# Kernel tuning notes

Hardware: AMD Instinct MI355X
Metric: run time of the kernel (lower is better)

The kernel has to match this reference:

```python
import jax, jax.numpy as jnp
import numpy as np

SPARSITY = 0.1
B, N, K = 256, 65536, 64

def setup_inputs() -> dict:
    key = jax.random.key(0)
    kx, kc = jax.random.split(key)
    x = jax.random.normal(kx, (B, N), dtype=jnp.float32)
    cluster_assignments = jax.random.randint(kc, (N,), 0, K, dtype=jnp.int32)
    cluster_weights = jnp.ones((K,), dtype=jnp.float32)
    return {"x": x, "cluster_weights": cluster_weights, "cluster_assignments": cluster_assignments}

def reference(x, cluster_weights, cluster_assignments):
    b, n = x.shape
    k = cluster_weights.shape[0]
    # cluster activation prob (context=None path): softmax(weights), same for all batch rows
    p = jax.nn.softmax(cluster_weights) * SPARSITY                      # [K]
    ku, kv = jax.random.split(jax.random.key(42))
    u = jax.random.uniform(ku, (b, n))   # drives the random permutation per (batch, cluster)
    v = jax.random.uniform(kv, (b, n))   # drives the binomial count (sum of Bernoullis)
    # Binomial(len(cluster_i), p_i) == sum of per-neuron Bernoulli(p_i) over the cluster
    bern = (v < p[cluster_assignments][None, :]).astype(jnp.int32)      # [B, N]
    counts = jax.vmap(lambda row: jax.ops.segment_sum(row, cluster_assignments, num_segments=k))(bern)  # [B, K]
    counts = jnp.maximum(counts, 1)                                     # max(1, binomial sample)
    # within-cluster uniform-random ranking: sort by (cluster, u); rank = pos - cluster_start
    sizes = jnp.bincount(cluster_assignments, length=k)                 # [K]
    starts = jnp.cumsum(sizes) - sizes                                  # exclusive cumsum [K]
    cluster_sorted = jnp.sort(cluster_assignments)                      # [N], batch-independent
    pos_in_cluster = jnp.arange(n) - starts[cluster_sorted]             # [N]
    keys = cluster_assignments.astype(jnp.float32)[None, :] + u * 0.999  # cluster-major composite key
    order = jnp.argsort(keys, axis=1)                                   # [B, N]
    mask_sorted = (pos_in_cluster[None, :] < counts[:, cluster_sorted]).astype(x.dtype)  # [B, N]
    mask = jnp.zeros_like(x).at[jnp.arange(b)[:, None], order].set(mask_sorted)
    return x * mask
```

## Files before the change

kernel.cpp:

```cpp
#include <hip/hip_runtime.h>
#include <stdint.h>

#define NROWS 256
#define NCOLS 65536
#define KCL   64
#define TMAX  20
#define NBLK  128
#define CHUNK (NCOLS / NBLK)
#define ZBLK  2048

__device__ __forceinline__ void tf2x32(uint32_t k0, uint32_t k1,
                                       uint32_t x0, uint32_t x1,
                                       uint32_t& o0, uint32_t& o1) {
  const uint32_t ks2 = k0 ^ k1 ^ 0x1BD11BDAu;
  x0 += k0; x1 += k1;
#define TFR(r) { x0 += x1; x1 = __builtin_rotateleft32(x1, (r)); x1 ^= x0; }
  TFR(13) TFR(15) TFR(26) TFR(6)
  x0 += k1; x1 += ks2 + 1u;
  TFR(17) TFR(29) TFR(16) TFR(24)
  x0 += ks2; x1 += k0 + 2u;
  TFR(13) TFR(15) TFR(26) TFR(6)
  x0 += k0; x1 += k1 + 3u;
  TFR(17) TFR(29) TFR(16) TFR(24)
  x0 += k1; x1 += ks2 + 4u;
  TFR(13) TFR(15) TFR(26) TFR(6)
  x0 += ks2; x1 += k0 + 5u;
#undef TFR
  o0 = x0; o1 = x1;
}

__device__ __forceinline__ uint32_t jax_bits(uint32_t k0, uint32_t k1, uint32_t f) {
  uint32_t o0, o1;
  tf2x32(k0, k1, 0u, f, o0, o1);
  return o0 ^ o1;
}

__device__ __forceinline__ float bits_to_u01(uint32_t bits) {
  return __uint_as_float((bits >> 9) | 0x3f800000u) - 1.0f;
}

__device__ __forceinline__ float key_from_ubits(uint32_t ubits, float kf) {
  return __fadd_rn(kf, __fmul_rn(bits_to_u01(ubits), 0.999f));
}

__device__ __forceinline__ int wave_sum_i(int v) {
  v += __builtin_amdgcn_update_dpp(0, v, 0xB1,  0xF, 0xF, true);
  v += __builtin_amdgcn_update_dpp(0, v, 0x4E,  0xF, 0xF, true);
  v += __builtin_amdgcn_update_dpp(0, v, 0x141, 0xF, 0xF, true);
  v += __builtin_amdgcn_update_dpp(0, v, 0x140, 0xF, 0xF, true);
  v += __builtin_amdgcn_ds_swizzle(v, 0x401F);
  v += __shfl_xor(v, 32, 64);
  return v;
}
__device__ __forceinline__ uint32_t wave_min_u(uint32_t v) {
  uint32_t o;
  o = (uint32_t)__builtin_amdgcn_update_dpp(0, (int)v, 0xB1,  0xF, 0xF, true); v = (o < v) ? o : v;
  o = (uint32_t)__builtin_amdgcn_update_dpp(0, (int)v, 0x4E,  0xF, 0xF, true); v = (o < v) ? o : v;
  o = (uint32_t)__builtin_amdgcn_update_dpp(0, (int)v, 0x141, 0xF, 0xF, true); v = (o < v) ? o : v;
  o = (uint32_t)__builtin_amdgcn_update_dpp(0, (int)v, 0x140, 0xF, 0xF, true); v = (o < v) ? o : v;
  o = (uint32_t)__builtin_amdgcn_ds_swizzle((int)v, 0x401F);                   v = (o < v) ? o : v;
  o = (uint32_t)__shfl_xor((int)v, 32, 64);                                    v = (o < v) ? o : v;
  return v;
}
__device__ __forceinline__ int wave_min_i(int v) {
  return (int)wave_min_u((uint32_t)v);
}

__global__ __launch_bounds__(256)
void k_zerohist(float4* __restrict__ outv, const int* __restrict__ a,
                int* __restrict__ blockhist) {
  const int gtid = blockIdx.x * 256 + threadIdx.x;
  const float4 z = make_float4(0.f, 0.f, 0.f, 0.f);
#pragma unroll
  for (int i = 0; i < 8; ++i)
    outv[gtid + i * (ZBLK * 256)] = z;
  if (blockIdx.x < NBLK) {
    __shared__ int h[KCL];
    if (threadIdx.x < KCL) h[threadIdx.x] = 0;
    __syncthreads();
    const int base = blockIdx.x * CHUNK;
#pragma unroll
    for (int i = base + threadIdx.x; i < base + CHUNK; i += 256)
      atomicAdd(&h[a[i]], 1);
    __syncthreads();
    if (threadIdx.x < KCL) blockhist[blockIdx.x * KCL + threadIdx.x] = h[threadIdx.x];
  }
}

__global__ void k_prefix_setup(int* __restrict__ blockhist, int* __restrict__ sizes,
                               int* __restrict__ starts,
                               const float* __restrict__ w, uint32_t* __restrict__ hdr,
                               uint32_t* __restrict__ vthresh) {
  const int k = threadIdx.x;
  int acc = 0;
#pragma unroll 8
  for (int blk = 0; blk < NBLK; ++blk) {
    const int t = blockhist[blk * KCL + k];
    blockhist[blk * KCL + k] = acc;
    acc += t;
  }
  sizes[k] = acc;
  int scan = acc;
#pragma unroll
  for (int d = 1; d < 64; d <<= 1) {
    const int o = __shfl_up(scan, d, 64);
    if (k >= d) scan += o;
  }
  starts[k] = scan - acc;
  const float wk = w[k];
  float m = wk;
#pragma unroll
  for (int d = 1; d < 64; d <<= 1) m = fmaxf(m, __shfl_xor(m, d, 64));
  const float e = expf(wk - m);
  float s = e;
#pragma unroll
  for (int d = 1; d < 64; d <<= 1) s += __shfl_xor(s, d, 64);
  const float pk = (e / s) * 0.1f;
  vthresh[k] = (uint32_t)ceilf(pk * 8388608.0f);
  if (k == 0) {
    uint32_t o0, o1;
    tf2x32(0u, 42u, 0u, 0u, o0, o1); hdr[0] = o0; hdr[1] = o1;
    tf2x32(0u, 42u, 0u, 1u, o0, o1); hdr[2] = o0; hdr[3] = o1;
  }
}

__global__ __launch_bounds__(256)
void k_scatter(const int* __restrict__ a, const int* __restrict__ blockhist,
               const int* __restrict__ starts, int* __restrict__ idx_sorted) {
  __shared__ int cur[KCL];
  const int tid = threadIdx.x;
  if (tid < KCL) cur[tid] = starts[tid] + blockhist[blockIdx.x * KCL + tid];
  __syncthreads();
  const int base = blockIdx.x * CHUNK;
#pragma unroll
  for (int i = base + tid; i < base + CHUNK; i += 256) {
    const int k = a[i];
    const int slot = atomicAdd(&cur[k], 1);
    idx_sorted[slot] = i;
  }
}

__global__ __launch_bounds__(256)
void k_select(const float* __restrict__ x,
              const int* __restrict__ idx_sorted,
              const int* __restrict__ sizes,
              const int* __restrict__ starts,
              const uint32_t* __restrict__ hdr,
              const uint32_t* __restrict__ vthresh,
              float* __restrict__ out) {
  __shared__ uint32_t kbs[TMAX][256];
  const int tid = threadIdx.x;
  const int lane = tid & 63;
  const int wid = tid >> 6;
  const int k = blockIdx.x >> 6;
  const int b = ((blockIdx.x & 63) << 2) | wid;

  int sz = sizes[k];
  const int st = starts[k];
  if (sz <= 0) return;
  if (sz > TMAX * 64) sz = TMAX * 64;

  const uint32_t ku0 = hdr[0], ku1 = hdr[1], kv0 = hdr[2], kv1 = hdr[3];
  const uint32_t vt = vthresh[k];
  const float kf = (float)k;
  const uint32_t bbase = (uint32_t)(b << 16);

  const int full = sz >> 6;
  const int rem  = sz & 63;
  const int tcap = full + (rem ? 1 : 0);

  uint32_t curmin = 0xFFFFFFFFu;
  int cnt = 0;
#pragma unroll 4
  for (int t = 0; t < full; ++t) {
    const int nv = idx_sorted[st + lane + (t << 6)];
    const uint32_t f = bbase + (uint32_t)nv;
    const uint32_t ubv = jax_bits(ku0, ku1, f);
    const uint32_t vbv = jax_bits(kv0, kv1, f);
    cnt += ((vbv >> 9) < vt) ? 1 : 0;
    const uint32_t kbv = __float_as_uint(key_from_ubits(ubv, kf));
    kbs[t][tid] = kbv;
    curmin = (kbv < curmin) ? kbv : curmin;
  }
  if (rem) {
    uint32_t kbv = 0xFFFFFFFFu;
    if (lane < rem) {
      const int nv = idx_sorted[st + (full << 6) + lane];
      const uint32_t f = bbase + (uint32_t)nv;
      const uint32_t ubv = jax_bits(ku0, ku1, f);
      const uint32_t vbv = jax_bits(kv0, kv1, f);
      cnt += ((vbv >> 9) < vt) ? 1 : 0;
      kbv = __float_as_uint(key_from_ubits(ubv, kf));
    }
    kbs[full][tid] = kbv;
    curmin = (kbv < curmin) ? kbv : curmin;
  }

  int C = wave_sum_i(cnt);
  if (C < 1) C = 1;

  uint32_t consumed = 0;
  uint32_t Tkey;
  for (int e = 0;; ++e) {
    const uint32_t wmn = wave_min_u(curmin);
    if (e == C - 1) { Tkey = wmn; break; }
    const unsigned long long bal = __ballot(curmin == wmn);
    const int src = (int)__ffsll((long long)bal) - 1;
    if (lane == src) {
      int ct = -1;
      for (int t = 0; t < tcap; ++t)
        if (ct < 0 && !((consumed >> t) & 1u) && kbs[t][tid] == wmn) ct = t;
      consumed |= (1u << ct);
      uint32_t nm = 0xFFFFFFFFu;
      for (int t = 0; t < tcap; ++t) {
        const uint32_t v = ((consumed >> t) & 1u) ? 0xFFFFFFFFu : kbs[t][tid];
        nm = (v < nm) ? v : nm;
      }
      curmin = nm;
    }
  }

  int packed = 0;
  for (int t = 0; t < tcap; ++t) {
    const uint32_t v = kbs[t][tid];
    packed += (v < Tkey) ? (1 << 16) : 0;
    packed += (v == Tkey) ? 1 : 0;
  }
  const int sred = wave_sum_i(packed);
  const int nbelow = sred >> 16;
  const int tieCnt = sred & 0xFFFF;
  const int r = C - nbelow;

  int cutN = 0x7FFFFFFF;
  if (r < tieCnt) {
    uint32_t cons2 = 0;
    for (int e = 0; e < r; ++e) {
      int mnN = 0x7FFFFFFF, mnT = 0;
      for (int t = 0; t < tcap; ++t) {
        if (kbs[t][tid] == Tkey && !((cons2 >> t) & 1u)) {
          const int n = idx_sorted[st + lane + (t << 6)];
          if (n < mnN) { mnN = n; mnT = t; }
        }
      }
      const int w = wave_min_i(mnN);
      cutN = w;
      const unsigned long long bal = __ballot(mnN == w);
      const int src = (int)__ffsll((long long)bal) - 1;
      if (lane == src) cons2 |= (1u << mnT);
    }
  }

  const size_t rowoff = (size_t)b * NCOLS;
  const bool allTies = (r >= tieCnt);
  for (int t = 0; t < tcap; ++t) {
    const uint32_t v = kbs[t][tid];
    bool sel = (v < Tkey);
    if (!sel && v == Tkey) {
      if (allTies) {
        sel = true;
      } else {
        const int n = idx_sorted[st + lane + (t << 6)];
        sel = (n <= cutN);
      }
    }
    if (sel) {
      const int n = idx_sorted[st + lane + (t << 6)];
      const size_t off = rowoff + (uint32_t)n;
      out[off] = x[off];
    }
  }
}

extern "C" void kernel_launch(void* const* d_in, const int* in_sizes, int n_in,
                              void* d_out, int out_size, void* d_ws, size_t ws_size,
                              hipStream_t stream) {
  const float* x = (const float*)d_in[0];
  const float* w = (const float*)d_in[1];
  const int* assign = (const int*)d_in[2];
  float* out = (float*)d_out;
  uint32_t* ws = (uint32_t*)d_ws;

  uint32_t* hdr       = ws;
  uint32_t* vthresh   = ws + 4;
  int*      sizes     = (int*)(ws + 68);
  int*      starts    = (int*)(ws + 132);
  int*      blockhist = (int*)(ws + 196);
  int*      idxs      = (int*)(ws + 196 + NBLK * KCL);

  k_zerohist<<<ZBLK, 256, 0, stream>>>((float4*)out, assign, blockhist);
  k_prefix_setup<<<1, 64, 0, stream>>>(blockhist, sizes, starts, w, hdr, vthresh);
  k_scatter<<<NBLK, 256, 0, stream>>>(assign, blockhist, starts, idxs);
  k_select<<<(NROWS * KCL) / 4, 256, 0, stream>>>(x, idxs, sizes, starts, hdr, vthresh, out);
  (void)n_in; (void)in_sizes; (void)ws_size;
}
```

Baseline: 112.6 us.

## Split key generation into a separate fully parallel kernel before selection

Moves the Threefry random-bit generation out of the per-(cluster,row) selection kernel into a new k_genkeys kernel. That kernel writes sorted-order keys and Bernoulli ballot bitmasks for all rows to workspace, and k_pick then reads them back and counts with popcount. The intent is to spread the hash-heavy work evenly across all lanes instead of across unevenly sized cluster waves. In exchange it adds a 64MB key buffer write and read plus an extra launch. The old path is kept as a fallback when the workspace is too small.

```diff
diff --git a/kernel.cpp b/kernel.cpp
--- a/kernel.cpp
+++ b/kernel.cpp
@@ -8,6 +8,7 @@
 #define NBLK  128
 #define CHUNK (NCOLS / NBLK)
 #define ZBLK  2048
+#define BCH   16
 
 __device__ __forceinline__ void tf2x32(uint32_t k0, uint32_t k1,
                                        uint32_t x0, uint32_t x1,
@@ -126,7 +127,8 @@
 
 __global__ __launch_bounds__(256)
 void k_scatter(const int* __restrict__ a, const int* __restrict__ blockhist,
-               const int* __restrict__ starts, int* __restrict__ idx_sorted) {
+               const int* __restrict__ starts, int* __restrict__ idx_sorted,
+               int* __restrict__ kq) {
   __shared__ int cur[KCL];
   const int tid = threadIdx.x;
   if (tid < KCL) cur[tid] = starts[tid] + blockhist[blockIdx.x * KCL + tid];
@@ -137,17 +139,49 @@
     const int k = a[i];
     const int slot = atomicAdd(&cur[k], 1);
     idx_sorted[slot] = i;
+    if (kq) kq[slot] = k;
   }
 }
 
 __global__ __launch_bounds__(256)
-void k_select(const float* __restrict__ x,
-              const int* __restrict__ idx_sorted,
-              const int* __restrict__ sizes,
-              const int* __restrict__ starts,
-              const uint32_t* __restrict__ hdr,
-              const uint32_t* __restrict__ vthresh,
-              float* __restrict__ out) {
+void k_genkeys(const int* __restrict__ idx_sorted, const int* __restrict__ kq,
+               const uint32_t* __restrict__ vthresh, const uint32_t* __restrict__ hdr,
+               uint32_t* __restrict__ keys, unsigned long long* __restrict__ bm) {
+  const int tid = threadIdx.x;
+  const int lane = tid & 63;
+  const int wavegid = blockIdx.x * 4 + (tid >> 6);
+  const int qt = wavegid >> 4;
+  const int b0 = (wavegid & 15) * BCH;
+
+  const int q = (qt << 6) + lane;
+  const int nv = idx_sorted[q];
+  const int kqv = kq[q];
+  const uint32_t vt = vthresh[kqv];
+  const float kf = (float)kqv;
+  const uint32_t ku0 = hdr[0], ku1 = hdr[1], kv0 = hdr[2], kv1 = hdr[3];
+
+  uint32_t f = ((uint32_t)b0 << 16) + (uint32_t)nv;
+  uint32_t kidx = ((uint32_t)b0 << 16) + (uint32_t)q;
+  size_t bmi = ((size_t)b0 << 10) + qt;
+#pragma unroll 4
+  for (int bi = 0; bi < BCH; ++bi) {
+    const uint32_t ubv = jax_bits(ku0, ku1, f);
+    const uint32_t vbv = jax_bits(kv0, kv1, f);
+    keys[kidx] = __float_as_uint(key_from_ubits(ubv, kf));
+    const unsigned long long bal = __ballot((vbv >> 9) < vt);
+    if (lane == 0) bm[bmi] = bal;
+    f += 65536u; kidx += 65536u; bmi += 1024;
+  }
+}
+
+__global__ __launch_bounds__(256)
+void k_pick(const float* __restrict__ x,
+            const uint32_t* __restrict__ keys,
+            const unsigned long long* __restrict__ bm,
+            const int* __restrict__ idx_sorted,
+            const int* __restrict__ sizes,
+            const int* __restrict__ starts,
+            float* __restrict__ out) {
   __shared__ uint32_t kbs[TMAX][256];
   const int tid = threadIdx.x;
   const int lane = tid & 63;
@@ -160,42 +194,33 @@
   if (sz <= 0) return;
   if (sz > TMAX * 64) sz = TMAX * 64;
 
-  const uint32_t ku0 = hdr[0], ku1 = hdr[1], kv0 = hdr[2], kv1 = hdr[3];
-  const uint32_t vt = vthresh[k];
-  const float kf = (float)k;
-  const uint32_t bbase = (uint32_t)(b << 16);
-
   const int full = sz >> 6;
   const int rem  = sz & 63;
   const int tcap = full + (rem ? 1 : 0);
+  const uint32_t* krow = keys + (((size_t)b) << 16) + st;
 
   uint32_t curmin = 0xFFFFFFFFu;
-  int cnt = 0;
 #pragma unroll 4
   for (int t = 0; t < full; ++t) {
-    const int nv = idx_sorted[st + lane + (t << 6)];
-    const uint32_t f = bbase + (uint32_t)nv;
-    const uint32_t ubv = jax_bits(ku0, ku1, f);
-    const uint32_t vbv = jax_bits(kv0, kv1, f);
-    cnt += ((vbv >> 9) < vt) ? 1 : 0;
-    const uint32_t kbv = __float_as_uint(key_from_ubits(ubv, kf));
-    kbs[t][tid] = kbv;
-    curmin = (kbv < curmin) ? kbv : curmin;
+    const uint32_t v = krow[lane + (t << 6)];
+    kbs[t][tid] = v;
+    curmin = (v < curmin) ? v : curmin;
   }
   if (rem) {
-    uint32_t kbv = 0xFFFFFFFFu;
-    if (lane < rem) {
-      const int nv = idx_sorted[st + (full << 6) + lane];
-      const uint32_t f = bbase + (uint32_t)nv;
-      const uint32_t ubv = jax_bits(ku0, ku1, f);
-      const uint32_t vbv = jax_bits(kv0, kv1, f);
-      cnt += ((vbv >> 9) < vt) ? 1 : 0;
-      kbv = __float_as_uint(key_from_ubits(ubv, kf));
-    }
-    kbs[full][tid] = kbv;
-    curmin = (kbv < curmin) ? kbv : curmin;
-  }
-
+    const uint32_t v = (lane < rem) ? krow[(full << 6) + lane] : 0xFFFFFFFFu;
+    kbs[full][tid] = v;
+    curmin = (v < curmin) ? v : curmin;
+  }
+
+  const int w0 = st >> 6, wl = (st + sz - 1) >> 6;
+  const int nw = wl - w0 + 1;
+  int cnt = 0;
+  if (lane < nw) {
+    unsigned long long m = bm[(((size_t)b) << 10) + w0 + lane];
+    if (lane == 0)      m &= (0xFFFFFFFFFFFFFFFFull << (st & 63));
+    if (lane == nw - 1) m &= ((2ull << ((st + sz - 1) & 63)) - 1ull);
+    cnt = __popcll(m);
+  }
   int C = wave_sum_i(cnt);
   if (C < 1) C = 1;
 
@@ -271,6 +296,137 @@
   }
 }
 
+__global__ __launch_bounds__(256)
+void k_select(const float* __restrict__ x,
+              const int* __restrict__ idx_sorted,
+              const int* __restrict__ sizes,
+              const int* __restrict__ starts,
+              const uint32_t* __restrict__ hdr,
+              const uint32_t* __restrict__ vthresh,
+              float* __restrict__ out) {
+  __shared__ uint32_t kbs[TMAX][256];
+  const int tid = threadIdx.x;
+  const int lane = tid & 63;
+  const int wid = tid >> 6;
+  const int k = blockIdx.x >> 6;
+  const int b = ((blockIdx.x & 63) << 2) | wid;
+
+  int sz = sizes[k];
+  const int st = starts[k];
+  if (sz <= 0) return;
+  if (sz > TMAX * 64) sz = TMAX * 64;
+
+  const uint32_t ku0 = hdr[0], ku1 = hdr[1], kv0 = hdr[2], kv1 = hdr[3];
+  const uint32_t vt = vthresh[k];
+  const float kf = (float)k;
+  const uint32_t bbase = (uint32_t)(b << 16);
+
+  const int full = sz >> 6;
+  const int rem  = sz & 63;
+  const int tcap = full + (rem ? 1 : 0);
+
+  uint32_t curmin = 0xFFFFFFFFu;
+  int cnt = 0;
+#pragma unroll 4
+  for (int t = 0; t < full; ++t) {
+    const int nv = idx_sorted[st + lane + (t << 6)];
+    const uint32_t f = bbase + (uint32_t)nv;
+    const uint32_t ubv = jax_bits(ku0, ku1, f);
+    const uint32_t vbv = jax_bits(kv0, kv1, f);
+    cnt += ((vbv >> 9) < vt) ? 1 : 0;
+    const uint32_t kbv = __float_as_uint(key_from_ubits(ubv, kf));
+    kbs[t][tid] = kbv;
+    curmin = (kbv < curmin) ? kbv : curmin;
+  }
+  if (rem) {
+    uint32_t kbv = 0xFFFFFFFFu;
+    if (lane < rem) {
+      const int nv = idx_sorted[st + (full << 6) + lane];
+      const uint32_t f = bbase + (uint32_t)nv;
+      const uint32_t ubv = jax_bits(ku0, ku1, f);
+      const uint32_t vbv = jax_bits(kv0, kv1, f);
+      cnt += ((vbv >> 9) < vt) ? 1 : 0;
+      kbv = __float_as_uint(key_from_ubits(ubv, kf));
+    }
+    kbs[full][tid] = kbv;
+    curmin = (kbv < curmin) ? kbv : curmin;
+  }
+
+  int C = wave_sum_i(cnt);
+  if (C < 1) C = 1;
+
+  uint32_t consumed = 0;
+  uint32_t Tkey;
+  for (int e = 0;; ++e) {
+    const uint32_t wmn = wave_min_u(curmin);
+    if (e == C - 1) { Tkey = wmn; break; }
+    const unsigned long long bal = __ballot(curmin == wmn);
+    const int src = (int)__ffsll((long long)bal) - 1;
+    if (lane == src) {
+      int ct = -1;
+      for (int t = 0; t < tcap; ++t)
+        if (ct < 0 && !((consumed >> t) & 1u) && kbs[t][tid] == wmn) ct = t;
+      consumed |= (1u << ct);
+      uint32_t nm = 0xFFFFFFFFu;
+      for (int t = 0; t < tcap; ++t) {
+        const uint32_t v = ((consumed >> t) & 1u) ? 0xFFFFFFFFu : kbs[t][tid];
+        nm = (v < nm) ? v : nm;
+      }
+      curmin = nm;
+    }
+  }
+
+  int packed = 0;
+  for (int t = 0; t < tcap; ++t) {
+    const uint32_t v = kbs[t][tid];
+    packed += (v < Tkey) ? (1 << 16) : 0;
+    packed += (v == Tkey) ? 1 : 0;
+  }
+  const int sred = wave_sum_i(packed);
+  const int nbelow = sred >> 16;
+  const int tieCnt = sred & 0xFFFF;
+  const int r = C - nbelow;
+
+  int cutN = 0x7FFFFFFF;
+  if (r < tieCnt) {
+    uint32_t cons2 = 0;
+    for (int e = 0; e < r; ++e) {
+      int mnN = 0x7FFFFFFF, mnT = 0;
+      for (int t = 0; t < tcap; ++t) {
+        if (kbs[t][tid] == Tkey && !((cons2 >> t) & 1u)) {
+          const int n = idx_sorted[st + lane + (t << 6)];
+          if (n < mnN) { mnN = n; mnT = t; }
+        }
+      }
+      const int w = wave_min_i(mnN);
+      cutN = w;
+      const unsigned long long bal = __ballot(mnN == w);
+      const int src = (int)__ffsll((long long)bal) - 1;
+      if (lane == src) cons2 |= (1u << mnT);
+    }
+  }
+
+  const size_t rowoff = (size_t)b * NCOLS;
+  const bool allTies = (r >= tieCnt);
+  for (int t = 0; t < tcap; ++t) {
+    const uint32_t v = kbs[t][tid];
+    bool sel = (v < Tkey);
+    if (!sel && v == Tkey) {
+      if (allTies) {
+        sel = true;
+      } else {
+        const int n = idx_sorted[st + lane + (t << 6)];
+        sel = (n <= cutN);
+      }
+    }
+    if (sel) {
+      const int n = idx_sorted[st + lane + (t << 6)];
+      const size_t off = rowoff + (uint32_t)n;
+      out[off] = x[off];
+    }
+  }
+}
+
 extern "C" void kernel_launch(void* const* d_in, const int* in_sizes, int n_in,
                               void* d_out, int out_size, void* d_ws, size_t ws_size,
                               hipStream_t stream) {
@@ -280,16 +436,39 @@
   float* out = (float*)d_out;
   uint32_t* ws = (uint32_t*)d_ws;
 
-  uint32_t* hdr       = ws;
-  uint32_t* vthresh   = ws + 4;
-  int*      sizes     = (int*)(ws + 68);
-  int*      starts    = (int*)(ws + 132);
-  int*      blockhist = (int*)(ws + 196);
-  int*      idxs      = (int*)(ws + 196 + NBLK * KCL);
+  const size_t U_HDR = 0;
+  const size_t U_VT  = 4;
+  const size_t U_SZ  = 68;
+  const size_t U_ST  = 132;
+  const size_t U_BH  = 196;
+  const size_t U_IDX = U_BH + NBLK * KCL;
+  const size_t U_KQ  = U_IDX + NCOLS;
+  const size_t U_BM  = U_KQ + NCOLS;
+  const size_t U_KEY = U_BM + 2 * NROWS * 1024;
+  const size_t U_END = U_KEY + (size_t)NROWS * NCOLS;
+
+  uint32_t* hdr       = ws + U_HDR;
+  uint32_t* vthresh   = ws + U_VT;
+  int*      sizes     = (int*)(ws + U_SZ);
+  int*      starts    = (int*)(ws + U_ST);
+  int*      blockhist = (int*)(ws + U_BH);
+  int*      idxs      = (int*)(ws + U_IDX);
+  int*      kq        = (int*)(ws + U_KQ);
+  unsigned long long* bm = (unsigned long long*)(ws + U_BM);
+  uint32_t* keys      = ws + U_KEY;
+
+  const bool split = (ws_size >= U_END * sizeof(uint32_t));
 
   k_zerohist<<<ZBLK, 256, 0, stream>>>((float4*)out, assign, blockhist);
   k_prefix_setup<<<1, 64, 0, stream>>>(blockhist, sizes, starts, w, hdr, vthresh);
-  k_scatter<<<NBLK, 256, 0, stream>>>(assign, blockhist, starts, idxs);
-  k_select<<<(NROWS * KCL) / 4, 256, 0, stream>>>(x, idxs, sizes, starts, hdr, vthresh, out);
-  (void)n_in; (void)in_sizes; (void)ws_size;
-}
+  k_scatter<<<NBLK, 256, 0, stream>>>(assign, blockhist, starts, idxs,
+                                      split ? kq : nullptr);
+  if (split) {
+    k_genkeys<<<4096, 256, 0, stream>>>(idxs, kq, vthresh, hdr, keys, bm);
+    k_pick<<<4096, 256, 0, stream>>>(x, keys, bm, idxs, sizes, starts, out);
+  } else {
+    k_select<<<(NROWS * KCL) / 4, 256, 0, stream>>>(x, idxs, sizes, starts, hdr,
+                                                    vthresh, out);
+  }
+  (void)n_in; (void)in_sizes;
+}
```

New measurement: 147.2 us. 1.31x slower.
